# Kernel optimization log

Hardware: AMD Instinct MI355X
Metric: run time of the kernel (lower is better)

Reference implementation:

```python
import jax, jax.numpy as jnp
import numpy as np

B, N, C, H, MC, LIE, KD = 2, 2048, 256, 8, 256, 3, 16
DH = C // H

def swish(x):
    return x * jax.nn.sigmoid(x)

def layernorm(x, g, b):
    m = jnp.mean(x, axis=-1, keepdims=True)
    v = jnp.var(x, axis=-1, keepdims=True)
    return (x - m) * jax.lax.rsqrt(v + 1e-5) * g + b

def setup_inputs():
    ks = jax.random.split(jax.random.key(0), 12)
    p = lambda i, shape, s: jax.random.normal(ks[i], shape, jnp.float32) * s
    return dict(
        pairwise_g=jax.random.normal(ks[0], (B, N, N, LIE), jnp.float32),
        x=jax.random.normal(ks[1], (B, N, C), jnp.float32),
        mask=jnp.ones((B, N), dtype=bool),
        ln1_g=jnp.ones((C,), jnp.float32), ln1_b=jnp.zeros((C,), jnp.float32),
        ln2_g=jnp.ones((C,), jnp.float32), ln2_b=jnp.zeros((C,), jnp.float32),
        wn_w1=p(2, (LIE, KD), 0.3), wn_b1=jnp.zeros((KD,), jnp.float32),
        wn_w2=p(3, (KD, KD), 0.3), wn_b2=jnp.zeros((KD,), jnp.float32),
        wn_w3=p(4, (KD, H), 0.3), wn_b3=jnp.zeros((H,), jnp.float32),
        wq=p(5, (C, C), 0.05), bq=jnp.zeros((C,), jnp.float32),
        wk=p(6, (C, C), 0.05), bk=jnp.zeros((C,), jnp.float32),
        in_w=p(7, (C, C), 0.05), in_b=jnp.zeros((C,), jnp.float32),
        out_w=p(8, (C, C), 0.05), out_b=jnp.zeros((C,), jnp.float32),
        mlp_w1=p(9, (C, C), 0.05), mlp_b1=jnp.zeros((C,), jnp.float32),
        mlp_w2=p(10, (C, C), 0.05), mlp_b2=jnp.zeros((C,), jnp.float32),
    )

def _ema(pairwise_g, x, mask, wn_w1, wn_b1, wn_w2, wn_b2, wn_w3, wn_b3,
         wq, bq, wk, bk, in_w, in_b, out_w, out_b):
    b, n, c = x.shape
    # neighbourhood extraction: topk smallest T(3) group distances (mc_samples=MC, fill=1.0)
    dists = jnp.linalg.norm(pairwise_g, axis=-1)                      # (b,n,n)
    dists = jnp.where(mask[:, None, :], dists, jnp.float32(1e8))
    _, idx = jax.lax.top_k(-dists, MC)                                # (b,n,k)
    nbhd_g = jnp.take_along_axis(pairwise_g, idx[..., None], axis=2)  # (b,n,k,LIE)
    nbhd_mask = jnp.take_along_axis(jnp.broadcast_to(mask[:, None, :], (b, n, n)), idx, axis=2)
    # location kernel: MultiheadWeightNet MLP on pairwise group elements -> per-head scalar
    hloc = swish(nbhd_g @ wn_w1 + wn_b1)
    hloc = swish(hloc @ wn_w2 + wn_b2)
    loc = hloc @ wn_w3 + wn_b3                                        # (b,n,k,H)
    # feature kernel: multihead dot product over gathered neighbour keys
    q = (x @ wq + bq).reshape(b, n, H, DH)
    kf = (x @ wk + bk).reshape(b, n, H, DH)
    k_nbhd = jax.vmap(lambda kfb, ib: kfb[ib])(kf, idx)               # (b,n,k,H,DH)
    scores = jnp.einsum('bnhd,bnkhd->bnkh', q, k_nbhd) / jnp.sqrt(jnp.float32(DH))
    pre = jnp.where(nbhd_mask[..., None], loc + scores, jnp.float32(-1e38))
    attn = jax.nn.softmax(pre, axis=2)                                # (b,n,k,H)
    # values; scatter attention into dense (b,n,n,H) exactly as the torch code, then aggregate
    v = (x @ in_w + in_b).reshape(b, n, H, DH)
    BS = jnp.arange(b)[:, None, None]
    NNS = jnp.arange(n)[None, :, None]
    aw = jnp.zeros((b, n, n, H), attn.dtype).at[BS, NNS, idx].set(attn)
    out = jnp.einsum('bnmh,bmhd->bnhd', aw, v).reshape(b, n, c)
    return out @ out_w + out_b

def reference(pairwise_g, x, mask, ln1_g, ln1_b, ln2_g, ln2_b,
              wn_w1, wn_b1, wn_w2, wn_b2, wn_w3, wn_b3,
              wq, bq, wk, bk, in_w, in_b, out_w, out_b,
              mlp_w1, mlp_b1, mlp_w2, mlp_b2):
    # EquivariantTransformerBlock with block_norm='layer_pre'
    x = x + _ema(pairwise_g, layernorm(x, ln1_g, ln1_b), mask,
                 wn_w1, wn_b1, wn_w2, wn_b2, wn_w3, wn_b3,
                 wq, bq, wk, bk, in_w, in_b, out_w, out_b)
    h = layernorm(x, ln2_g, ln2_b)
    x = x + (swish(h @ mlp_w1 + mlp_b1) @ mlp_w2 + mlp_b2)
    return x
```

## Files before the change

kernel.cpp:

```cpp
#include <hip/hip_runtime.h>
#include <hip/hip_bf16.h>

#define Bb 2
#define Nn 2048
#define Cc 256
#define Hh 8
#define MCk 256
#define RT (Bb * Nn)

typedef __hip_bfloat16 bf16;
typedef _Float16 f16;
typedef __fp16 h2v __attribute__((ext_vector_type(2)));
typedef __fp16 h8 __attribute__((ext_vector_type(8)));
typedef float f32x4 __attribute__((ext_vector_type(4)));

__device__ __forceinline__ h2v bc16(unsigned u) { return __builtin_bit_cast(h2v, u); }
__device__ __forceinline__ unsigned bcu(h2v v) { return __builtin_bit_cast(unsigned, v); }

__device__ __forceinline__ float dot2(h2v a, h2v b, float c) {
  return __builtin_amdgcn_fdot2(a, b, c, false);
}
__device__ __forceinline__ f32x4 mfma16(h8 a, h8 b, f32x4 c) {
  return __builtin_amdgcn_mfma_f32_16x16x32_f16(a, b, c, 0, 0, 0);
}
__device__ __forceinline__ float swish_f(float z) {
  return z * __builtin_amdgcn_rcpf(1.f + __expf(-z));
}

__global__ __launch_bounds__(256) void k1_prep_ln_select(
    const float* __restrict__ w0, const float* __restrict__ w1,
    const float* __restrict__ w2, const float* __restrict__ w3,
    const float* __restrict__ w4, const float* __restrict__ w5,
    f16* __restrict__ wtout,
    const float* __restrict__ x, const float* __restrict__ g,
    const float* __restrict__ b, f16* __restrict__ lnout,
    const float* __restrict__ pg, int* __restrict__ idxout)
{
  __shared__ float tile[32][33];
  __shared__ int rc[31][4];
  __shared__ int eqlist[2048];
  __shared__ int nsel, neq;
  int bx = blockIdx.x;
  int t = threadIdx.x;
  if (bx < 384) {
    int wb = bx / 64, tid = bx % 64;
    const float* ws_[6] = {w0, w1, w2, w3, w4, w5};
    const float* W = ws_[wb];
    f16* o = wtout + (size_t)wb * 65536;
    int tn0 = (tid & 7) * 32, tk0 = (tid >> 3) * 32;
    int tl = t & 31, tg = t >> 5;
#pragma unroll
    for (int r = 0; r < 4; r++) {
      int k = tk0 + tg * 4 + r;
      tile[tg * 4 + r][tl] = W[(size_t)k * 256 + tn0 + tl];
    }
    __syncthreads();
#pragma unroll
    for (int r = 0; r < 4; r++) {
      int n = tn0 + tg * 4 + r;
      o[(size_t)n * 256 + tk0 + tl] = (f16)tile[tl][tg * 4 + r];
    }
  } else if (bx < 1408) {
    int wave = t >> 6, lane = t & 63;
    int row = (bx - 384) * 4 + wave;
    const float4 v = reinterpret_cast<const float4*>(x + (size_t)row * Cc)[lane];
    float s  = v.x + v.y + v.z + v.w;
    float s2 = v.x * v.x + v.y * v.y + v.z * v.z + v.w * v.w;
#pragma unroll
    for (int m = 1; m < 64; m <<= 1) {
      s  += __shfl_xor(s, m);
      s2 += __shfl_xor(s2, m);
    }
    float mean = s * (1.0f / Cc);
    float var  = s2 * (1.0f / Cc) - mean * mean;
    float rs   = rsqrtf(var + 1e-5f);
    const float4 gg = reinterpret_cast<const float4*>(g)[lane];
    const float4 bb = reinterpret_cast<const float4*>(b)[lane];
    float ox = (v.x - mean) * rs * gg.x + bb.x;
    float oy = (v.y - mean) * rs * gg.y + bb.y;
    float oz = (v.z - mean) * rs * gg.z + bb.z;
    float ow = (v.w - mean) * rs * gg.w + bb.w;
    uint2 st;
    st.x = bcu(__builtin_amdgcn_cvt_pkrtz(ox, oy));
    st.y = bcu(__builtin_amdgcn_cvt_pkrtz(oz, ow));
    *(uint2*)(lnout + (size_t)row * Cc + lane * 4) = st;
  } else {
    int row = bx - 1408;
    int wave = t >> 6, lane = t & 63;
    const float4* b4 = (const float4*)(pg + (size_t)row * (Nn * 3));
    float4 v0 = b4[6 * t + 0], v1 = b4[6 * t + 1], v2 = b4[6 * t + 2];
    float4 v3 = b4[6 * t + 3], v4 = b4[6 * t + 4], v5 = b4[6 * t + 5];
    unsigned u[8];
    u[0] = __float_as_uint(sqrtf(v0.x * v0.x + v0.y * v0.y + v0.z * v0.z));
    u[1] = __float_as_uint(sqrtf(v0.w * v0.w + v1.x * v1.x + v1.y * v1.y));
    u[2] = __float_as_uint(sqrtf(v1.z * v1.z + v1.w * v1.w + v2.x * v2.x));
    u[3] = __float_as_uint(sqrtf(v2.y * v2.y + v2.z * v2.z + v2.w * v2.w));
    u[4] = __float_as_uint(sqrtf(v3.x * v3.x + v3.y * v3.y + v3.z * v3.z));
    u[5] = __float_as_uint(sqrtf(v3.w * v3.w + v4.x * v4.x + v4.y * v4.y));
    u[6] = __float_as_uint(sqrtf(v4.z * v4.z + v4.w * v4.w + v5.x * v5.x));
    u[7] = __float_as_uint(sqrtf(v5.y * v5.y + v5.z * v5.z + v5.w * v5.w));
    if (t == 0) { nsel = 0; neq = 0; }
    unsigned T = 0;
    for (int bit = 30; bit >= 0; bit--) {
      unsigned cand = T | (1u << bit);
      int c = 0;
#pragma unroll
      for (int jj = 0; jj < 8; jj++) c += __popcll(__ballot(u[jj] < cand));
      if (lane == 0) rc[bit][wave] = c;
      __syncthreads();
      c = rc[bit][0] + rc[bit][1] + rc[bit][2] + rc[bit][3];
      if (c <= MCk - 1) T = cand;
    }
    unsigned long long lmask = (1ull << lane) - 1ull;
#pragma unroll
    for (int jj = 0; jj < 8; jj++) {
      int col = t * 8 + jj;
      bool less = u[jj] < T;
      bool eq   = (u[jj] == T);
      unsigned long long bls = __ballot(less);
      unsigned long long beq = __ballot(eq);
      int cls = __popcll(bls), ceq = __popcll(beq);
      int bl_ = 0, be_ = 0;
      if (lane == 0) {
        bl_ = atomicAdd(&nsel, cls);
        be_ = atomicAdd(&neq, ceq);
      }
      bl_ = __shfl(bl_, 0);
      be_ = __shfl(be_, 0);
      if (less) idxout[(size_t)row * MCk + bl_ + __popcll(bls & lmask)] = col;
      if (eq)   eqlist[be_ + __popcll(beq & lmask)] = col;
    }
    __syncthreads();
    int cl = nsel, nq = neq;
    int need = MCk - cl;
    for (int e = t; e < nq; e += 256) {
      int colE = eqlist[e];
      int rank = 0;
      for (int j = 0; j < nq; j++) rank += (eqlist[j] < colE) ? 1 : 0;
      if (rank < need) idxout[(size_t)row * MCk + cl + rank] = colE;
    }
  }
}

__global__ __launch_bounds__(256) void k2_locmlp_qkv(
    const float* __restrict__ pg, const int* __restrict__ idxb,
    uint4* __restrict__ locout,
    const float* __restrict__ w1, const float* __restrict__ b1,
    const float* __restrict__ w2, const float* __restrict__ b2,
    const float* __restrict__ w3, const float* __restrict__ b3,
    const f16* __restrict__ A,
    const f16* __restrict__ WTq, const float* __restrict__ Bq,
    const f16* __restrict__ WTk, const float* __restrict__ Bk,
    const f16* __restrict__ WTv, const float* __restrict__ Bv,
    f16* __restrict__ outq, f16* __restrict__ outk, f16* __restrict__ outv)
{
  __shared__ float wnl[64];
  __shared__ h2v   w2p[128];
  __shared__ float bn2[16];
  __shared__ h2v   w3p[64];
  __shared__ float bn3[8];
  int t = threadIdx.x;
  if (blockIdx.x < 4096) {
    int row = blockIdx.x;
    for (int i = t; i < 280; i += 256) {
      if (i < 48) {
        wnl[i] = w1[i];
      } else if (i < 64) {
        wnl[i] = b1[i - 48];
      } else if (i < 192) {
        int j = i - 64, i2 = j >> 4, o = j & 15;
        w2p[j] = __builtin_amdgcn_cvt_pkrtz(w2[(2 * i2) * 16 + o], w2[(2 * i2 + 1) * 16 + o]);
      } else if (i < 208) {
        bn2[i - 192] = b2[i - 192];
      } else if (i < 272) {
        int j = i - 208, i2 = j >> 3, o = j & 7;
        w3p[j] = __builtin_amdgcn_cvt_pkrtz(w3[(2 * i2) * 8 + o], w3[(2 * i2 + 1) * 8 + o]);
      } else {
        bn3[i - 272] = b3[i - 272];
      }
    }
    int m = idxb[(size_t)row * 256 + t];
    const float* gsp = pg + ((size_t)row * Nn + m) * 3;
    float g0 = gsp[0], g1 = gsp[1], g2 = gsp[2];
    __syncthreads();
    float h1[16];
#pragma unroll
    for (int o = 0; o < 16; o++) {
      float z = wnl[48 + o] + g0 * wnl[o] + g1 * wnl[16 + o] + g2 * wnl[32 + o];
      h1[o] = swish_f(z);
    }
    h2v hp1[8];
#pragma unroll
    for (int i = 0; i < 8; i++) hp1[i] = __builtin_amdgcn_cvt_pkrtz(h1[2 * i], h1[2 * i + 1]);
    float hh[16];
#pragma unroll
    for (int o = 0; o < 16; o++) {
      float z = bn2[o];
#pragma unroll
      for (int i2 = 0; i2 < 8; i2++) z = dot2(hp1[i2], w2p[i2 * 16 + o], z);
      hh[o] = swish_f(z);
    }
    h2v hp2[8];
#pragma unroll
    for (int i = 0; i < 8; i++) hp2[i] = __builtin_amdgcn_cvt_pkrtz(hh[2 * i], hh[2 * i + 1]);
    float loc[8];
#pragma unroll
    for (int o = 0; o < 8; o++) {
      float z = bn3[o];
#pragma unroll
      for (int i2 = 0; i2 < 8; i2++) z = dot2(hp2[i2], w3p[i2 * 8 + o], z);
      loc[o] = z;
    }
    uint4 lv;
    lv.x = bcu(__builtin_amdgcn_cvt_pkrtz(loc[0], loc[1]));
    lv.y = bcu(__builtin_amdgcn_cvt_pkrtz(loc[2], loc[3]));
    lv.z = bcu(__builtin_amdgcn_cvt_pkrtz(loc[4], loc[5]));
    lv.w = bcu(__builtin_amdgcn_cvt_pkrtz(loc[6], loc[7]));
    locout[(size_t)row * 256 + t] = lv;
  } else {
    int bxq = blockIdx.x - 4096;
    int wid = t >> 6, lane = t & 63;
    int m0 = ((bxq & 63) * 4 + wid) * 16;
    int n0 = (bxq >> 6) * 32;
    int lm = lane & 15, lk = lane >> 4;
    const h8* Ab = (const h8*)(A + (size_t)(m0 + lm) * 256) + lk;
    const h8* Q0 = (const h8*)(WTq + (size_t)(n0 + lm) * 256) + lk;
    const h8* Q1 = (const h8*)(WTq + (size_t)(n0 + 16 + lm) * 256) + lk;
    const h8* K0 = (const h8*)(WTk + (size_t)(n0 + lm) * 256) + lk;
    const h8* K1 = (const h8*)(WTk + (size_t)(n0 + 16 + lm) * 256) + lk;
    const h8* V0 = (const h8*)(WTv + (size_t)(n0 + lm) * 256) + lk;
    const h8* V1 = (const h8*)(WTv + (size_t)(n0 + 16 + lm) * 256) + lk;
    f32x4 aq0 = {0.f,0.f,0.f,0.f}, aq1 = {0.f,0.f,0.f,0.f};
    f32x4 ak0 = {0.f,0.f,0.f,0.f}, ak1 = {0.f,0.f,0.f,0.f};
    f32x4 av0 = {0.f,0.f,0.f,0.f}, av1 = {0.f,0.f,0.f,0.f};
#pragma unroll
    for (int ks = 0; ks < 8; ks++) {
      h8 a = Ab[ks * 4];
      aq0 = mfma16(a, Q0[ks * 4], aq0);
      aq1 = mfma16(a, Q1[ks * 4], aq1);
      ak0 = mfma16(a, K0[ks * 4], ak0);
      ak1 = mfma16(a, K1[ks * 4], ak1);
      av0 = mfma16(a, V0[ks * 4], av0);
      av1 = mfma16(a, V1[ks * 4], av1);
    }
    const float qs = 0.17677669529663687f;
    float bq0 = Bq[n0 + lm], bq1 = Bq[n0 + 16 + lm];
    float bk0 = Bk[n0 + lm], bk1 = Bk[n0 + 16 + lm];
    float bv0 = Bv[n0 + lm], bv1 = Bv[n0 + 16 + lm];
#pragma unroll
    for (int i = 0; i < 4; i++) {
      size_t row = m0 + lk * 4 + i;
      outq[row * 256 + n0 + lm]      = (f16)((aq0[i] + bq0) * qs);
      outq[row * 256 + n0 + 16 + lm] = (f16)((aq1[i] + bq1) * qs);
      outk[row * 256 + n0 + lm]      = (f16)(ak0[i] + bk0);
      outk[row * 256 + n0 + 16 + lm] = (f16)(ak1[i] + bk1);
      outv[row * 256 + n0 + lm]      = (f16)(av0[i] + bv0);
      outv[row * 256 + n0 + 16 + lm] = (f16)(av1[i] + bv1);
    }
  }
}

__global__ __launch_bounds__(256, 4) void attn_kernel(
    const f16* __restrict__ qh, const f16* __restrict__ kh,
    const f16* __restrict__ vv, const int* __restrict__ idxb,
    const uint4* __restrict__ loc16, f16* __restrict__ out)
{
  __shared__ int   offs[256];
  __shared__ float ps[256 * 9];
  __shared__ float agg[4 * 256];
  __shared__ float redmx[4][8];
  __shared__ float redsm[4][8];
  int t = threadIdx.x;
  int row = blockIdx.x;
  int bidx = row >> 11;
  int g = t >> 5, c = t & 31;

  int m = idxb[(size_t)row * 256 + t];
  offs[t] = (bidx * Nn + m) * 512;
  const uint4 qu = *(const uint4*)((const char*)qh + (size_t)row * 512 + (size_t)c * 16);
  h2v q0 = bc16(qu.x), q1 = bc16(qu.y), q2 = bc16(qu.z), q3 = bc16(qu.w);
  const uint4 lv = loc16[(size_t)row * 256 + t];
  __syncthreads();

  int offr[32];
#pragma unroll
  for (int kk = 0; kk < 32; kk++) offr[kk] = offs[kk * 8 + g];

  const char* kbase = (const char*)kh + (size_t)c * 16;
#pragma unroll
  for (int kk = 0; kk < 32; kk += 4) {
    const uint4 k0 = *(const uint4*)(kbase + offr[kk + 0]);
    const uint4 k1 = *(const uint4*)(kbase + offr[kk + 1]);
    const uint4 k2 = *(const uint4*)(kbase + offr[kk + 2]);
    const uint4 k3 = *(const uint4*)(kbase + offr[kk + 3]);
    float p0 = dot2(bc16(k0.x), q0, 0.f);
    float p1 = dot2(bc16(k1.x), q0, 0.f);
    float p2 = dot2(bc16(k2.x), q0, 0.f);
    float p3 = dot2(bc16(k3.x), q0, 0.f);
    p0 = dot2(bc16(k0.y), q1, p0); p1 = dot2(bc16(k1.y), q1, p1);
    p2 = dot2(bc16(k2.y), q1, p2); p3 = dot2(bc16(k3.y), q1, p3);
    p0 = dot2(bc16(k0.z), q2, p0); p1 = dot2(bc16(k1.z), q2, p1);
    p2 = dot2(bc16(k2.z), q2, p2); p3 = dot2(bc16(k3.z), q2, p3);
    p0 = dot2(bc16(k0.w), q3, p0); p1 = dot2(bc16(k1.w), q3, p1);
    p2 = dot2(bc16(k2.w), q3, p2); p3 = dot2(bc16(k3.w), q3, p3);
    p0 += __shfl_xor(p0, 1); p1 += __shfl_xor(p1, 1);
    p2 += __shfl_xor(p2, 1); p3 += __shfl_xor(p3, 1);
    p0 += __shfl_xor(p0, 2); p1 += __shfl_xor(p1, 2);
    p2 += __shfl_xor(p2, 2); p3 += __shfl_xor(p3, 2);
    if ((c & 3) == 0) {
      int hh_ = c >> 2;
      ps[((kk + 0) * 8 + g) * 9 + hh_] = p0;
      ps[((kk + 1) * 8 + g) * 9 + hh_] = p1;
      ps[((kk + 2) * 8 + g) * 9 + hh_] = p2;
      ps[((kk + 3) * 8 + g) * 9 + hh_] = p3;
    }
  }
  __syncthreads();

  h2v l01 = bc16(lv.x), l23 = bc16(lv.y), l45 = bc16(lv.z), l67 = bc16(lv.w);
  float pre[8];
  pre[0] = ps[t * 9 + 0] + (float)l01.x;
  pre[1] = ps[t * 9 + 1] + (float)l01.y;
  pre[2] = ps[t * 9 + 2] + (float)l23.x;
  pre[3] = ps[t * 9 + 3] + (float)l23.y;
  pre[4] = ps[t * 9 + 4] + (float)l45.x;
  pre[5] = ps[t * 9 + 5] + (float)l45.y;
  pre[6] = ps[t * 9 + 6] + (float)l67.x;
  pre[7] = ps[t * 9 + 7] + (float)l67.y;
  float mx[8];
#pragma unroll
  for (int h = 0; h < 8; h++) mx[h] = pre[h];
#pragma unroll
  for (int mm = 1; mm < 64; mm <<= 1) {
#pragma unroll
    for (int h = 0; h < 8; h++) mx[h] = fmaxf(mx[h], __shfl_xor(mx[h], mm));
  }
  int wv = t >> 6, ln = t & 63;
  if (ln == 0) {
#pragma unroll
    for (int h = 0; h < 8; h++) redmx[wv][h] = mx[h];
  }
  __syncthreads();
#pragma unroll
  for (int h = 0; h < 8; h++)
    mx[h] = fmaxf(fmaxf(redmx[0][h], redmx[1][h]), fmaxf(redmx[2][h], redmx[3][h]));
  float e[8], sm[8];
#pragma unroll
  for (int h = 0; h < 8; h++) { e[h] = __expf(pre[h] - mx[h]); sm[h] = e[h]; }
#pragma unroll
  for (int mm = 1; mm < 64; mm <<= 1) {
#pragma unroll
    for (int h = 0; h < 8; h++) sm[h] += __shfl_xor(sm[h], mm);
  }
  if (ln == 0) {
#pragma unroll
    for (int h = 0; h < 8; h++) redsm[wv][h] = sm[h];
  }
  __syncthreads();
#pragma unroll
  for (int h = 0; h < 8; h++) {
    float ssum = redsm[0][h] + redsm[1][h] + redsm[2][h] + redsm[3][h];
    ps[t * 9 + h] = e[h] * __builtin_amdgcn_rcpf(ssum);
  }
  __syncthreads();

  h2v ac0 = {0, 0}, ac1 = {0, 0}, ac2 = {0, 0}, ac3 = {0, 0};
  const char* vbase = (const char*)vv + (size_t)c * 16;
  int hh_ = c >> 2;
#pragma unroll
  for (int kk = 0; kk < 32; kk += 4) {
    const uint4 v0 = *(const uint4*)(vbase + offr[kk + 0]);
    const uint4 v1 = *(const uint4*)(vbase + offr[kk + 1]);
    const uint4 v2 = *(const uint4*)(vbase + offr[kk + 2]);
    const uint4 v3 = *(const uint4*)(vbase + offr[kk + 3]);
    float aw0 = ps[((kk + 0) * 8 + g) * 9 + hh_];
    float aw1 = ps[((kk + 1) * 8 + g) * 9 + hh_];
    float aw2 = ps[((kk + 2) * 8 + g) * 9 + hh_];
    float aw3 = ps[((kk + 3) * 8 + g) * 9 + hh_];
    h2v w0 = __builtin_amdgcn_cvt_pkrtz(aw0, aw0);
    h2v w1 = __builtin_amdgcn_cvt_pkrtz(aw1, aw1);
    h2v w2 = __builtin_amdgcn_cvt_pkrtz(aw2, aw2);
    h2v w3 = __builtin_amdgcn_cvt_pkrtz(aw3, aw3);
    ac0 = bc16(v0.x) * w0 + ac0; ac1 = bc16(v0.y) * w0 + ac1;
    ac2 = bc16(v0.z) * w0 + ac2; ac3 = bc16(v0.w) * w0 + ac3;
    ac0 = bc16(v1.x) * w1 + ac0; ac1 = bc16(v1.y) * w1 + ac1;
    ac2 = bc16(v1.z) * w1 + ac2; ac3 = bc16(v1.w) * w1 + ac3;
    ac0 = bc16(v2.x) * w2 + ac0; ac1 = bc16(v2.y) * w2 + ac1;
    ac2 = bc16(v2.z) * w2 + ac2; ac3 = bc16(v2.w) * w2 + ac3;
    ac0 = bc16(v3.x) * w3 + ac0; ac1 = bc16(v3.y) * w3 + ac1;
    ac2 = bc16(v3.z) * w3 + ac2; ac3 = bc16(v3.w) * w3 + ac3;
  }
  float acc[8] = {(float)ac0.x, (float)ac0.y, (float)ac1.x, (float)ac1.y,
                  (float)ac2.x, (float)ac2.y, (float)ac3.x, (float)ac3.y};
#pragma unroll
  for (int i = 0; i < 8; i++) acc[i] += __shfl_xor(acc[i], 32);
  if ((t & 32) == 0) {
#pragma unroll
    for (int i = 0; i < 8; i++) agg[wv * 256 + c * 8 + i] = acc[i];
  }
  __syncthreads();
  float o = agg[t] + agg[256 + t] + agg[512 + t] + agg[768 + t];
  out[(size_t)row * 256 + t] = (f16)o;
}

__global__ __launch_bounds__(512) void epilogue(
    const f16* __restrict__ A, const f16* __restrict__ WTo,
    const float* __restrict__ bo, const float* __restrict__ xres,
    const float* __restrict__ g, const float* __restrict__ b,
    const f16* __restrict__ WT1, const float* __restrict__ b1,
    const f16* __restrict__ WT2, const float* __restrict__ b2,
    float* __restrict__ outp)
{
  __shared__ float sred[8][16][2];
  __shared__ f16 hl[16 * 272];
  __shared__ f16 hl2[16 * 272];
  int wid = threadIdx.x >> 6, lane = threadIdx.x & 63;
  int lm = lane & 15, lk = lane >> 4;
  int m0 = blockIdx.x * 16;
  int c0 = wid * 32 + lm, c1 = c0 + 16;

  const h8* Ab  = (const h8*)(A + (size_t)(m0 + lm) * 256) + lk;
  const h8* Bo0 = (const h8*)(WTo + (size_t)c0 * 256) + lk;
  const h8* Bo1 = (const h8*)(WTo + (size_t)c1 * 256) + lk;
  f32x4 ac0 = {0,0,0,0}, ac1 = {0,0,0,0};
#pragma unroll
  for (int ks = 0; ks < 8; ks++) {
    h8 a = Ab[ks * 4];
    ac0 = mfma16(a, Bo0[ks * 4], ac0);
    ac1 = mfma16(a, Bo1[ks * 4], ac1);
  }
  float bo0 = bo[c0], bo1 = bo[c1];
  float xr0[4], xr1[4];
  float s[4], s2[4];
#pragma unroll
  for (int i = 0; i < 4; i++) {
    size_t row = m0 + lk * 4 + i;
    float y0 = ac0[i] + bo0 + xres[row * 256 + c0];
    float y1 = ac1[i] + bo1 + xres[row * 256 + c1];
    xr0[i] = y0; xr1[i] = y1;
    s[i] = y0 + y1; s2[i] = y0 * y0 + y1 * y1;
  }
#pragma unroll
  for (int mm = 1; mm < 16; mm <<= 1) {
#pragma unroll
    for (int i = 0; i < 4; i++) {
      s[i]  += __shfl_xor(s[i], mm);
      s2[i] += __shfl_xor(s2[i], mm);
    }
  }
  if (lm == 0) {
#pragma unroll
    for (int i = 0; i < 4; i++) {
      sred[wid][lk * 4 + i][0] = s[i];
      sred[wid][lk * 4 + i][1] = s2[i];
    }
  }
  __syncthreads();
  float g0 = g[c0], g1 = g[c1], bb0 = b[c0], bb1 = b[c1];
#pragma unroll
  for (int i = 0; i < 4; i++) {
    int r = lk * 4 + i;
    float ts = 0.f, ts2 = 0.f;
#pragma unroll
    for (int w = 0; w < 8; w++) { ts += sred[w][r][0]; ts2 += sred[w][r][1]; }
    float mean = ts * (1.f / 256.f);
    float var  = ts2 * (1.f / 256.f) - mean * mean;
    float rs   = rsqrtf(var + 1e-5f);
    hl[r * 272 + c0] = (f16)((xr0[i] - mean) * rs * g0 + bb0);
    hl[r * 272 + c1] = (f16)((xr1[i] - mean) * rs * g1 + bb1);
  }
  __syncthreads();

  const h8* B10 = (const h8*)(WT1 + (size_t)c0 * 256) + lk;
  const h8* B11 = (const h8*)(WT1 + (size_t)c1 * 256) + lk;
  f32x4 m10 = {0,0,0,0}, m11 = {0,0,0,0};
#pragma unroll
  for (int ks = 0; ks < 8; ks++) {
    h8 a2 = *(const h8*)&hl[lm * 272 + ks * 32 + lk * 8];
    m10 = mfma16(a2, B10[ks * 4], m10);
    m11 = mfma16(a2, B11[ks * 4], m11);
  }
  float b10 = b1[c0], b11 = b1[c1];
#pragma unroll
  for (int i = 0; i < 4; i++) {
    int r = lk * 4 + i;
    hl2[r * 272 + c0] = (f16)swish_f(m10[i] + b10);
    hl2[r * 272 + c1] = (f16)swish_f(m11[i] + b11);
  }
  __syncthreads();

  const h8* B20 = (const h8*)(WT2 + (size_t)c0 * 256) + lk;
  const h8* B21 = (const h8*)(WT2 + (size_t)c1 * 256) + lk;
  f32x4 o0 = {0,0,0,0}, o1 = {0,0,0,0};
#pragma unroll
  for (int ks = 0; ks < 8; ks++) {
    h8 a3 = *(const h8*)&hl2[lm * 272 + ks * 32 + lk * 8];
    o0 = mfma16(a3, B20[ks * 4], o0);
    o1 = mfma16(a3, B21[ks * 4], o1);
  }
  float b20 = b2[c0], b21 = b2[c1];
#pragma unroll
  for (int i = 0; i < 4; i++) {
    size_t row = m0 + lk * 4 + i;
    outp[row * 256 + c0] = o0[i] + b20 + xr0[i];
    outp[row * 256 + c1] = o1[i] + b21 + xr1[i];
  }
}

extern "C" void kernel_launch(void* const* d_in, const int* in_sizes, int n_in,
                              void* d_out, int out_size, void* d_ws, size_t ws_size,
                              hipStream_t stream)
{
  (void)in_sizes; (void)n_in; (void)out_size; (void)ws_size;
  const float* pg   = (const float*)d_in[0];
  const float* x    = (const float*)d_in[1];
  const float* ln1g = (const float*)d_in[3];
  const float* ln1b = (const float*)d_in[4];
  const float* ln2g = (const float*)d_in[5];
  const float* ln2b = (const float*)d_in[6];
  const float* wnw1 = (const float*)d_in[7];
  const float* wnb1 = (const float*)d_in[8];
  const float* wnw2 = (const float*)d_in[9];
  const float* wnb2 = (const float*)d_in[10];
  const float* wnw3 = (const float*)d_in[11];
  const float* wnb3 = (const float*)d_in[12];
  const float* wq   = (const float*)d_in[13];
  const float* bq   = (const float*)d_in[14];
  const float* wk   = (const float*)d_in[15];
  const float* bk   = (const float*)d_in[16];
  const float* inw  = (const float*)d_in[17];
  const float* inb  = (const float*)d_in[18];
  const float* outw = (const float*)d_in[19];
  const float* outbv= (const float*)d_in[20];
  const float* m1w  = (const float*)d_in[21];
  const float* m1b  = (const float*)d_in[22];
  const float* m2w  = (const float*)d_in[23];
  const float* m2b  = (const float*)d_in[24];

  const size_t RC = (size_t)RT * 256;
  f16*   WTall = (f16*)d_ws;
  f16*   WTq = WTall + 0 * 65536;
  f16*   WTk = WTall + 1 * 65536;
  f16*   WTv = WTall + 2 * 65536;
  f16*   WTo = WTall + 3 * 65536;
  f16*   WTm1= WTall + 4 * 65536;
  f16*   WTm2= WTall + 5 * 65536;
  f16*   ln1h = WTall + 6 * 65536;
  f16*   qh  = ln1h + RC;
  f16*   kh  = qh + RC;
  f16*   vvb = kh + RC;
  int*   idxb= (int*)(vvb + RC);
  f16*   emah= (f16*)(idxb + RC);
  uint4* loc16 = (uint4*)(emah + RC);

  dim3 blk(256);
  k1_prep_ln_select<<<dim3(384 + RT / 4 + RT), blk, 0, stream>>>(
      wq, wk, inw, outw, m1w, m2w, WTall, x, ln1g, ln1b, ln1h, pg, idxb);
  k2_locmlp_qkv<<<dim3(RT + 512), blk, 0, stream>>>(
      pg, idxb, loc16, wnw1, wnb1, wnw2, wnb2, wnw3, wnb3,
      ln1h, WTq, bq, WTk, bk, WTv, inb, qh, kh, vvb);
  attn_kernel<<<dim3(RT), blk, 0, stream>>>(qh, kh, vvb, idxb, loc16, emah);
  epilogue<<<dim3(RT / 16), dim3(512), 0, stream>>>(
      emah, WTo, outbv, x, ln2g, ln2b, WTm1, m1b, WTm2, m2b, (float*)d_out);
}
```

Baseline: 147.3 us.

## Split attention into separate score/softmax and value-aggregation kernels

The fused attention kernel becomes two kernels. The first computes the scores and softmax and writes fp16 attention weights over the location buffer in place. The second reloads the neighbour indices and weights and gathers V to aggregate. Both kernels also widen the gather batch from 4 to 8 loads, read offsets from shared memory instead of a 32-entry register array, and drop the explicit occupancy hint, all aimed at lower register pressure and more loads in flight. The cost is an extra launch, a round trip of the weights through global memory, and a second read of the index array.

```diff
diff --git a/kernel.cpp b/kernel.cpp
--- a/kernel.cpp
+++ b/kernel.cpp
@@ -260,14 +260,12 @@
   }
 }
 
-__global__ __launch_bounds__(256, 4) void attn_kernel(
+__global__ __launch_bounds__(256) void attn_score(
     const f16* __restrict__ qh, const f16* __restrict__ kh,
-    const f16* __restrict__ vv, const int* __restrict__ idxb,
-    const uint4* __restrict__ loc16, f16* __restrict__ out)
+    const int* __restrict__ idxb, uint4* __restrict__ loc_aw)
 {
   __shared__ int   offs[256];
   __shared__ float ps[256 * 9];
-  __shared__ float agg[4 * 256];
   __shared__ float redmx[4][8];
   __shared__ float redsm[4][8];
   int t = threadIdx.x;
@@ -279,40 +277,54 @@
   offs[t] = (bidx * Nn + m) * 512;
   const uint4 qu = *(const uint4*)((const char*)qh + (size_t)row * 512 + (size_t)c * 16);
   h2v q0 = bc16(qu.x), q1 = bc16(qu.y), q2 = bc16(qu.z), q3 = bc16(qu.w);
-  const uint4 lv = loc16[(size_t)row * 256 + t];
-  __syncthreads();
-
-  int offr[32];
-#pragma unroll
-  for (int kk = 0; kk < 32; kk++) offr[kk] = offs[kk * 8 + g];
+  const uint4 lv = loc_aw[(size_t)row * 256 + t];
+  __syncthreads();
 
   const char* kbase = (const char*)kh + (size_t)c * 16;
 #pragma unroll
-  for (int kk = 0; kk < 32; kk += 4) {
-    const uint4 k0 = *(const uint4*)(kbase + offr[kk + 0]);
-    const uint4 k1 = *(const uint4*)(kbase + offr[kk + 1]);
-    const uint4 k2 = *(const uint4*)(kbase + offr[kk + 2]);
-    const uint4 k3 = *(const uint4*)(kbase + offr[kk + 3]);
-    float p0 = dot2(bc16(k0.x), q0, 0.f);
-    float p1 = dot2(bc16(k1.x), q0, 0.f);
-    float p2 = dot2(bc16(k2.x), q0, 0.f);
-    float p3 = dot2(bc16(k3.x), q0, 0.f);
-    p0 = dot2(bc16(k0.y), q1, p0); p1 = dot2(bc16(k1.y), q1, p1);
-    p2 = dot2(bc16(k2.y), q1, p2); p3 = dot2(bc16(k3.y), q1, p3);
-    p0 = dot2(bc16(k0.z), q2, p0); p1 = dot2(bc16(k1.z), q2, p1);
-    p2 = dot2(bc16(k2.z), q2, p2); p3 = dot2(bc16(k3.z), q2, p3);
-    p0 = dot2(bc16(k0.w), q3, p0); p1 = dot2(bc16(k1.w), q3, p1);
-    p2 = dot2(bc16(k2.w), q3, p2); p3 = dot2(bc16(k3.w), q3, p3);
+  for (int kk = 0; kk < 32; kk += 8) {
+    uint4 k0 = *(const uint4*)(kbase + offs[(kk + 0) * 8 + g]);
+    uint4 k1 = *(const uint4*)(kbase + offs[(kk + 1) * 8 + g]);
+    uint4 k2 = *(const uint4*)(kbase + offs[(kk + 2) * 8 + g]);
+    uint4 k3 = *(const uint4*)(kbase + offs[(kk + 3) * 8 + g]);
+    uint4 k4 = *(const uint4*)(kbase + offs[(kk + 4) * 8 + g]);
+    uint4 k5 = *(const uint4*)(kbase + offs[(kk + 5) * 8 + g]);
+    uint4 k6 = *(const uint4*)(kbase + offs[(kk + 6) * 8 + g]);
+    uint4 k7 = *(const uint4*)(kbase + offs[(kk + 7) * 8 + g]);
+    float p0 = dot2(bc16(k0.x), q0, 0.f); p0 = dot2(bc16(k0.y), q1, p0);
+    p0 = dot2(bc16(k0.z), q2, p0); p0 = dot2(bc16(k0.w), q3, p0);
+    float p1 = dot2(bc16(k1.x), q0, 0.f); p1 = dot2(bc16(k1.y), q1, p1);
+    p1 = dot2(bc16(k1.z), q2, p1); p1 = dot2(bc16(k1.w), q3, p1);
+    float p2 = dot2(bc16(k2.x), q0, 0.f); p2 = dot2(bc16(k2.y), q1, p2);
+    p2 = dot2(bc16(k2.z), q2, p2); p2 = dot2(bc16(k2.w), q3, p2);
+    float p3 = dot2(bc16(k3.x), q0, 0.f); p3 = dot2(bc16(k3.y), q1, p3);
+    p3 = dot2(bc16(k3.z), q2, p3); p3 = dot2(bc16(k3.w), q3, p3);
+    float p4 = dot2(bc16(k4.x), q0, 0.f); p4 = dot2(bc16(k4.y), q1, p4);
+    p4 = dot2(bc16(k4.z), q2, p4); p4 = dot2(bc16(k4.w), q3, p4);
+    float p5 = dot2(bc16(k5.x), q0, 0.f); p5 = dot2(bc16(k5.y), q1, p5);
+    p5 = dot2(bc16(k5.z), q2, p5); p5 = dot2(bc16(k5.w), q3, p5);
+    float p6 = dot2(bc16(k6.x), q0, 0.f); p6 = dot2(bc16(k6.y), q1, p6);
+    p6 = dot2(bc16(k6.z), q2, p6); p6 = dot2(bc16(k6.w), q3, p6);
+    float p7 = dot2(bc16(k7.x), q0, 0.f); p7 = dot2(bc16(k7.y), q1, p7);
+    p7 = dot2(bc16(k7.z), q2, p7); p7 = dot2(bc16(k7.w), q3, p7);
     p0 += __shfl_xor(p0, 1); p1 += __shfl_xor(p1, 1);
     p2 += __shfl_xor(p2, 1); p3 += __shfl_xor(p3, 1);
+    p4 += __shfl_xor(p4, 1); p5 += __shfl_xor(p5, 1);
+    p6 += __shfl_xor(p6, 1); p7 += __shfl_xor(p7, 1);
     p0 += __shfl_xor(p0, 2); p1 += __shfl_xor(p1, 2);
     p2 += __shfl_xor(p2, 2); p3 += __shfl_xor(p3, 2);
+    p4 += __shfl_xor(p4, 2); p5 += __shfl_xor(p5, 2);
+    p6 += __shfl_xor(p6, 2); p7 += __shfl_xor(p7, 2);
     if ((c & 3) == 0) {
       int hh_ = c >> 2;
       ps[((kk + 0) * 8 + g) * 9 + hh_] = p0;
       ps[((kk + 1) * 8 + g) * 9 + hh_] = p1;
       ps[((kk + 2) * 8 + g) * 9 + hh_] = p2;
       ps[((kk + 3) * 8 + g) * 9 + hh_] = p3;
+      ps[((kk + 4) * 8 + g) * 9 + hh_] = p4;
+      ps[((kk + 5) * 8 + g) * 9 + hh_] = p5;
+      ps[((kk + 6) * 8 + g) * 9 + hh_] = p6;
+      ps[((kk + 7) * 8 + g) * 9 + hh_] = p7;
     }
   }
   __syncthreads();
@@ -357,30 +369,61 @@
     for (int h = 0; h < 8; h++) redsm[wv][h] = sm[h];
   }
   __syncthreads();
+  float w_[8];
 #pragma unroll
   for (int h = 0; h < 8; h++) {
     float ssum = redsm[0][h] + redsm[1][h] + redsm[2][h] + redsm[3][h];
-    ps[t * 9 + h] = e[h] * __builtin_amdgcn_rcpf(ssum);
-  }
+    w_[h] = e[h] * __builtin_amdgcn_rcpf(ssum);
+  }
+  uint4 ost;
+  ost.x = bcu(__builtin_amdgcn_cvt_pkrtz(w_[0], w_[1]));
+  ost.y = bcu(__builtin_amdgcn_cvt_pkrtz(w_[2], w_[3]));
+  ost.z = bcu(__builtin_amdgcn_cvt_pkrtz(w_[4], w_[5]));
+  ost.w = bcu(__builtin_amdgcn_cvt_pkrtz(w_[6], w_[7]));
+  loc_aw[(size_t)row * 256 + t] = ost;
+}
+
+__global__ __launch_bounds__(256) void attn_agg(
+    const f16* __restrict__ vv, const int* __restrict__ idxb,
+    const uint4* __restrict__ aw, f16* __restrict__ out)
+{
+  __shared__ int   offs[256];
+  __shared__ uint4 awl[256];
+  __shared__ float agg[4 * 256];
+  int t = threadIdx.x;
+  int row = blockIdx.x;
+  int bidx = row >> 11;
+  int g = t >> 5, c = t & 31;
+  int wv = t >> 6;
+
+  int m = idxb[(size_t)row * 256 + t];
+  offs[t] = (bidx * Nn + m) * 512;
+  awl[t]  = aw[(size_t)row * 256 + t];
   __syncthreads();
 
   h2v ac0 = {0, 0}, ac1 = {0, 0}, ac2 = {0, 0}, ac3 = {0, 0};
   const char* vbase = (const char*)vv + (size_t)c * 16;
   int hh_ = c >> 2;
 #pragma unroll
-  for (int kk = 0; kk < 32; kk += 4) {
-    const uint4 v0 = *(const uint4*)(vbase + offr[kk + 0]);
-    const uint4 v1 = *(const uint4*)(vbase + offr[kk + 1]);
-    const uint4 v2 = *(const uint4*)(vbase + offr[kk + 2]);
-    const uint4 v3 = *(const uint4*)(vbase + offr[kk + 3]);
-    float aw0 = ps[((kk + 0) * 8 + g) * 9 + hh_];
-    float aw1 = ps[((kk + 1) * 8 + g) * 9 + hh_];
-    float aw2 = ps[((kk + 2) * 8 + g) * 9 + hh_];
-    float aw3 = ps[((kk + 3) * 8 + g) * 9 + hh_];
-    h2v w0 = __builtin_amdgcn_cvt_pkrtz(aw0, aw0);
-    h2v w1 = __builtin_amdgcn_cvt_pkrtz(aw1, aw1);
-    h2v w2 = __builtin_amdgcn_cvt_pkrtz(aw2, aw2);
-    h2v w3 = __builtin_amdgcn_cvt_pkrtz(aw3, aw3);
+  for (int kk = 0; kk < 32; kk += 8) {
+    uint4 v0 = *(const uint4*)(vbase + offs[(kk + 0) * 8 + g]);
+    uint4 v1 = *(const uint4*)(vbase + offs[(kk + 1) * 8 + g]);
+    uint4 v2 = *(const uint4*)(vbase + offs[(kk + 2) * 8 + g]);
+    uint4 v3 = *(const uint4*)(vbase + offs[(kk + 3) * 8 + g]);
+    uint4 v4 = *(const uint4*)(vbase + offs[(kk + 4) * 8 + g]);
+    uint4 v5 = *(const uint4*)(vbase + offs[(kk + 5) * 8 + g]);
+    uint4 v6 = *(const uint4*)(vbase + offs[(kk + 6) * 8 + g]);
+    uint4 v7 = *(const uint4*)(vbase + offs[(kk + 7) * 8 + g]);
+    __fp16 f0 = ((const __fp16*)&awl[(kk + 0) * 8 + g])[hh_];
+    __fp16 f1 = ((const __fp16*)&awl[(kk + 1) * 8 + g])[hh_];
+    __fp16 f2 = ((const __fp16*)&awl[(kk + 2) * 8 + g])[hh_];
+    __fp16 f3 = ((const __fp16*)&awl[(kk + 3) * 8 + g])[hh_];
+    __fp16 f4 = ((const __fp16*)&awl[(kk + 4) * 8 + g])[hh_];
+    __fp16 f5 = ((const __fp16*)&awl[(kk + 5) * 8 + g])[hh_];
+    __fp16 f6 = ((const __fp16*)&awl[(kk + 6) * 8 + g])[hh_];
+    __fp16 f7 = ((const __fp16*)&awl[(kk + 7) * 8 + g])[hh_];
+    h2v w0 = {f0, f0}, w1 = {f1, f1}, w2 = {f2, f2}, w3 = {f3, f3};
+    h2v w4 = {f4, f4}, w5 = {f5, f5}, w6 = {f6, f6}, w7 = {f7, f7};
     ac0 = bc16(v0.x) * w0 + ac0; ac1 = bc16(v0.y) * w0 + ac1;
     ac2 = bc16(v0.z) * w0 + ac2; ac3 = bc16(v0.w) * w0 + ac3;
     ac0 = bc16(v1.x) * w1 + ac0; ac1 = bc16(v1.y) * w1 + ac1;
@@ -389,6 +432,14 @@
     ac2 = bc16(v2.z) * w2 + ac2; ac3 = bc16(v2.w) * w2 + ac3;
     ac0 = bc16(v3.x) * w3 + ac0; ac1 = bc16(v3.y) * w3 + ac1;
     ac2 = bc16(v3.z) * w3 + ac2; ac3 = bc16(v3.w) * w3 + ac3;
+    ac0 = bc16(v4.x) * w4 + ac0; ac1 = bc16(v4.y) * w4 + ac1;
+    ac2 = bc16(v4.z) * w4 + ac2; ac3 = bc16(v4.w) * w4 + ac3;
+    ac0 = bc16(v5.x) * w5 + ac0; ac1 = bc16(v5.y) * w5 + ac1;
+    ac2 = bc16(v5.z) * w5 + ac2; ac3 = bc16(v5.w) * w5 + ac3;
+    ac0 = bc16(v6.x) * w6 + ac0; ac1 = bc16(v6.y) * w6 + ac1;
+    ac2 = bc16(v6.z) * w6 + ac2; ac3 = bc16(v6.w) * w6 + ac3;
+    ac0 = bc16(v7.x) * w7 + ac0; ac1 = bc16(v7.y) * w7 + ac1;
+    ac2 = bc16(v7.z) * w7 + ac2; ac3 = bc16(v7.w) * w7 + ac3;
   }
   float acc[8] = {(float)ac0.x, (float)ac0.y, (float)ac1.x, (float)ac1.y,
                   (float)ac2.x, (float)ac2.y, (float)ac3.x, (float)ac3.y};
@@ -559,7 +610,8 @@
   k2_locmlp_qkv<<<dim3(RT + 512), blk, 0, stream>>>(
       pg, idxb, loc16, wnw1, wnb1, wnw2, wnb2, wnw3, wnb3,
       ln1h, WTq, bq, WTk, bk, WTv, inb, qh, kh, vvb);
-  attn_kernel<<<dim3(RT), blk, 0, stream>>>(qh, kh, vvb, idxb, loc16, emah);
+  attn_score<<<dim3(RT), blk, 0, stream>>>(qh, kh, idxb, loc16);
+  attn_agg<<<dim3(RT), blk, 0, stream>>>(vvb, idxb, loc16, emah);
   epilogue<<<dim3(RT / 16), dim3(512), 0, stream>>>(
       emah, WTo, outbv, x, ln2g, ln2b, WTm1, m1b, WTm2, m2b, (float*)d_out);
 }
```

Result: slower. 155.8 us (+5.8%).
